# Performance work log

Hardware: AMD Instinct MI355X
Metric: run time of the kernel (lower is better)

Reference implementation:

```python
import jax, jax.numpy as jnp
import numpy as np

N_ATOMS = 100000
N_EDGES = 625000
N_MOL = 1000
EMB_ATOM = 256
EMB_EDGE = 128


def setup_inputs() -> dict:
    key = jax.random.key(0)
    ks = jax.random.split(key, 8)
    h_energy = jax.random.normal(ks[0], (N_ATOMS, EMB_ATOM), dtype=jnp.float32)
    h_forces = jax.random.normal(ks[1], (N_EDGES, EMB_EDGE), dtype=jnp.float32)
    V_st = jax.random.normal(ks[2], (N_EDGES, 3), dtype=jnp.float32)
    idx_t = jax.random.randint(ks[3], (N_EDGES,), 0, N_ATOMS, dtype=jnp.int64)
    batch_idx = jnp.sort(jax.random.randint(ks[4], (N_ATOMS,), 0, N_MOL, dtype=jnp.int64))
    W_energy = jax.random.normal(ks[5], (EMB_ATOM, 1), dtype=jnp.float32) / np.sqrt(EMB_ATOM)
    W_forces = jax.random.normal(ks[6], (EMB_EDGE, 1), dtype=jnp.float32) / np.sqrt(EMB_EDGE)
    b_forces = jnp.zeros((1,), dtype=jnp.float32)
    return {
        "h_energy": h_energy,
        "h_forces": h_forces,
        "V_st": V_st,
        "idx_t": idx_t,
        "batch_idx": batch_idx,
        "W_energy": W_energy,
        "W_forces": W_forces,
        "b_forces": b_forces,
    }


def reference(h_energy, h_forces, V_st, idx_t, batch_idx, W_energy, W_forces, b_forces):
    # Energy head: per-atom linear (bias=False), scatter-sum over molecules.
    e_atom = h_energy @ W_energy                      # [N, 1]
    y = jax.ops.segment_sum(e_atom, batch_idx, num_segments=N_MOL)  # [B, 1]
    y = y[:, 0]                                       # rearrange 'b 1 -> b'
    # Forces head: per-edge linear, scale by unit edge vector V_st,
    # scatter-sum into target atoms idx_t.
    f_edge = (h_forces @ W_forces + b_forces) * V_st  # [E, 3] via broadcast of [E,1]
    force = jax.ops.segment_sum(f_edge, idx_t, num_segments=N_ATOMS)  # [N, 3]
    return y, force
```

## Files before the change

kernel.cpp:

```cpp
#include <hip/hip_runtime.h>

#define N_ATOMS 100000
#define N_EDGES 625000
#define N_MOL   1000
#define EMB_ATOM 256
#define EMB_EDGE 128

typedef float f32x4 __attribute__((ext_vector_type(4)));

__device__ __forceinline__ float dot4(f32x4 a, f32x4 b) {
    return a.x * b.x + a.y * b.y + a.z * b.z + a.w * b.w;
}

#define REP      8
#define YREP_STR 1024
#define FREP_OFF 8192
#define FREP_STR 300000
#define WS_FLOATS (FREP_OFF + REP * FREP_STR)

__global__ __launch_bounds__(256) void zero_kernel(f32x4* __restrict__ p, int n4)
{
    const int i = blockIdx.x * blockDim.x + threadIdx.x;
    if (i < n4) p[i] = (f32x4)(0.f, 0.f, 0.f, 0.f);
}

__global__ __launch_bounds__(256) void merge_kernel(
    const float* __restrict__ ws, float* __restrict__ out)
{
    const int i = blockIdx.x * blockDim.x + threadIdx.x;
    if (i >= 250 + 75000) return;
    const f32x4* w4 = reinterpret_cast<const f32x4*>(ws);
    f32x4*       o4 = reinterpret_cast<f32x4*>(out);
    if (i < 250) {
        f32x4 s = (f32x4)(0.f, 0.f, 0.f, 0.f);
        #pragma unroll
        for (int k = 0; k < REP; ++k) s += w4[i + k * (YREP_STR/4)];
        o4[i] = s;
    } else {
        const int j = i - 250;
        const f32x4* f4 = w4 + FREP_OFF/4;
        f32x4 s = (f32x4)(0.f, 0.f, 0.f, 0.f);
        #pragma unroll
        for (int k = 0; k < REP; ++k) s += f4[j + k * (FREP_STR/4)];
        o4[i] = s;
    }
}

#define FTILES  ((N_EDGES + 15) / 16)
#define FPBLOCKS 1960
#define ETILES  (N_ATOMS / 8)
#define EPBLOCKS 600

__global__ __launch_bounds__(256) void fused_kernel(
    const float* __restrict__ h_energy,
    const float* __restrict__ h_forces,
    const float* __restrict__ V_st,
    const int*   __restrict__ idx_t,
    const int*   __restrict__ batch_idx,
    const float* __restrict__ W_energy,
    const float* __restrict__ W_forces,
    const float* __restrict__ b_forces,
    float*       __restrict__ ws)
{
    const int lane = threadIdx.x & 63;

    if (blockIdx.x < FPBLOCKS) {
        const int wslot = blockIdx.x * 4 + (threadIdx.x >> 6);
        const int slot  = lane >> 3;
        const int sub   = lane & 7;

        const f32x4* wf   = reinterpret_cast<const f32x4*>(W_forces);
        const f32x4* base = reinterpret_cast<const f32x4*>(h_forces);
        float* frep = ws + FREP_OFF + (wslot & (REP-1)) * FREP_STR;

        f32x4 b0 = wf[sub + 0];
        f32x4 b1 = wf[sub + 8];
        f32x4 b2 = wf[sub + 16];
        f32x4 b3 = wf[sub + 24];
        const float bias = b_forces[0];

        for (int tile = wslot; tile < FTILES; tile += FPBLOCKS * 4) {
            #pragma unroll
            for (int g = 0; g < 2; ++g) {
                const int e = tile * 16 + g * 8 + slot;
                float s = 0.f;
                if (e < N_EDGES) {
                    const f32x4* row = base + (size_t)e * 32;
                    f32x4 a0 = __builtin_nontemporal_load(row + sub + 0);
                    f32x4 a1 = __builtin_nontemporal_load(row + sub + 8);
                    f32x4 a2 = __builtin_nontemporal_load(row + sub + 16);
                    f32x4 a3 = __builtin_nontemporal_load(row + sub + 24);
                    s = dot4(a0, b0) + dot4(a1, b1) + dot4(a2, b2) + dot4(a3, b3);
                }
                s += __shfl_xor(s, 1, 64);
                s += __shfl_xor(s, 2, 64);
                s += __shfl_xor(s, 4, 64);
                if (e < N_EDGES && sub < 3) {
                    const int   t = idx_t[e];
                    const float v = V_st[(size_t)e * 3 + sub];
                    atomicAdd(&frep[(size_t)t * 3 + sub], (s + bias) * v);
                }
            }
        }
    } else if (blockIdx.x < FPBLOCKS + EPBLOCKS) {
        const int wslot = (blockIdx.x - FPBLOCKS) * 4 + (threadIdx.x >> 6);
        const int slot  = lane >> 4;
        const int sub   = lane & 15;

        const f32x4* we   = reinterpret_cast<const f32x4*>(W_energy);
        const f32x4* base = reinterpret_cast<const f32x4*>(h_energy);
        float* yrep = ws + (wslot & (REP-1)) * YREP_STR;

        f32x4 b0 = we[sub + 0];
        f32x4 b1 = we[sub + 16];
        f32x4 b2 = we[sub + 32];
        f32x4 b3 = we[sub + 48];

        for (int tile = wslot; tile < ETILES; tile += EPBLOCKS * 4) {
            #pragma unroll
            for (int g = 0; g < 2; ++g) {
                const int a = tile * 8 + g * 4 + slot;
                const f32x4* row = base + (size_t)a * 64;
                f32x4 a0 = __builtin_nontemporal_load(row + sub + 0);
                f32x4 a1 = __builtin_nontemporal_load(row + sub + 16);
                f32x4 a2 = __builtin_nontemporal_load(row + sub + 32);
                f32x4 a3 = __builtin_nontemporal_load(row + sub + 48);
                float s = dot4(a0, b0) + dot4(a1, b1) + dot4(a2, b2) + dot4(a3, b3);

                s += __shfl_xor(s, 1, 64);
                s += __shfl_xor(s, 2, 64);
                s += __shfl_xor(s, 4, 64);
                s += __shfl_xor(s, 8, 64);

                if (sub == 0) atomicAdd(&yrep[batch_idx[a]], s);
            }
        }
    }
}

extern "C" void kernel_launch(void* const* d_in, const int* in_sizes, int n_in,
                              void* d_out, int out_size, void* d_ws, size_t ws_size,
                              hipStream_t stream) {
    const float* h_energy  = (const float*)d_in[0];
    const float* h_forces  = (const float*)d_in[1];
    const float* V_st      = (const float*)d_in[2];
    const int*   idx_t     = (const int*)d_in[3];
    const int*   batch_idx = (const int*)d_in[4];
    const float* W_energy  = (const float*)d_in[5];
    const float* W_forces  = (const float*)d_in[6];
    const float* b_forces  = (const float*)d_in[7];

    float* ws  = (float*)d_ws;
    float* out = (float*)d_out;

    const int zn4 = WS_FLOATS / 4;
    zero_kernel<<<(zn4 + 255) / 256, 256, 0, stream>>>((f32x4*)d_ws, zn4);

    fused_kernel<<<FPBLOCKS + EPBLOCKS, 256, 0, stream>>>(
        h_energy, h_forces, V_st, idx_t, batch_idx,
        W_energy, W_forces, b_forces, ws);

    merge_kernel<<<(75250 + 255) / 256, 256, 0, stream>>>(ws, out);
}
```

Measured before the change: 96.77 us.

## Software-pipeline row loads one tile ahead in both force and energy loops

Restructures both grid-stride loops so each wavefront prefetches the next tile's feature rows, indices and V_st values into registers while it reduces and atomically accumulates the current tile. Out-of-range edges are clamped to a valid row so loads are unconditional. The aim is to hide global memory latency behind the dot-product, shuffle and atomic work. The cost is roughly double the register footprint for row data, which may lower occupancy. Most waves run only about two or three iterations, so there is little to overlap.

```diff
diff --git a/kernel.cpp b/kernel.cpp
--- a/kernel.cpp
+++ b/kernel.cpp
@@ -46,10 +46,12 @@
     }
 }
 
-#define FTILES  ((N_EDGES + 15) / 16)
+#define FTILES   ((N_EDGES + 15) / 16)
 #define FPBLOCKS 1960
-#define ETILES  (N_ATOMS / 8)
+#define FSTRIDE  (FPBLOCKS * 4)
+#define ETILES   (N_ATOMS / 8)
 #define EPBLOCKS 600
+#define ESTRIDE  (EPBLOCKS * 4)
 
 __global__ __launch_bounds__(256) void fused_kernel(
     const float* __restrict__ h_energy,
@@ -79,28 +81,63 @@
         f32x4 b3 = wf[sub + 24];
         const float bias = b_forces[0];
 
-        for (int tile = wslot; tile < FTILES; tile += FPBLOCKS * 4) {
-            #pragma unroll
-            for (int g = 0; g < 2; ++g) {
-                const int e = tile * 16 + g * 8 + slot;
-                float s = 0.f;
-                if (e < N_EDGES) {
-                    const f32x4* row = base + (size_t)e * 32;
-                    f32x4 a0 = __builtin_nontemporal_load(row + sub + 0);
-                    f32x4 a1 = __builtin_nontemporal_load(row + sub + 8);
-                    f32x4 a2 = __builtin_nontemporal_load(row + sub + 16);
-                    f32x4 a3 = __builtin_nontemporal_load(row + sub + 24);
-                    s = dot4(a0, b0) + dot4(a1, b1) + dot4(a2, b2) + dot4(a3, b3);
+        f32x4 c[8]; int ct[2]; float cv[2]; bool cok[2];
+
+        int tile = wslot;
+        {
+            #pragma unroll
+            for (int g = 0; g < 2; ++g) {
+                const int e  = tile * 16 + g * 8 + slot;
+                cok[g] = (e < N_EDGES);
+                const int ec = cok[g] ? e : (N_EDGES - 1);
+                const f32x4* row = base + (size_t)ec * 32;
+                c[g*4+0] = __builtin_nontemporal_load(row + sub + 0);
+                c[g*4+1] = __builtin_nontemporal_load(row + sub + 8);
+                c[g*4+2] = __builtin_nontemporal_load(row + sub + 16);
+                c[g*4+3] = __builtin_nontemporal_load(row + sub + 24);
+                ct[g] = idx_t[ec];
+                cv[g] = V_st[(size_t)ec * 3 + (sub < 3 ? sub : 0)];
+            }
+        }
+
+        for (;;) {
+            const int next     = tile + FSTRIDE;
+            const bool has_next = (next < FTILES);
+
+            f32x4 n[8]; int nt[2]; float nv[2]; bool nok[2];
+            if (has_next) {
+                #pragma unroll
+                for (int g = 0; g < 2; ++g) {
+                    const int e  = next * 16 + g * 8 + slot;
+                    nok[g] = (e < N_EDGES);
+                    const int ec = nok[g] ? e : (N_EDGES - 1);
+                    const f32x4* row = base + (size_t)ec * 32;
+                    n[g*4+0] = __builtin_nontemporal_load(row + sub + 0);
+                    n[g*4+1] = __builtin_nontemporal_load(row + sub + 8);
+                    n[g*4+2] = __builtin_nontemporal_load(row + sub + 16);
+                    n[g*4+3] = __builtin_nontemporal_load(row + sub + 24);
+                    nt[g] = idx_t[ec];
+                    nv[g] = V_st[(size_t)ec * 3 + (sub < 3 ? sub : 0)];
                 }
+            }
+
+            #pragma unroll
+            for (int g = 0; g < 2; ++g) {
+                float s = dot4(c[g*4+0], b0) + dot4(c[g*4+1], b1)
+                        + dot4(c[g*4+2], b2) + dot4(c[g*4+3], b3);
                 s += __shfl_xor(s, 1, 64);
                 s += __shfl_xor(s, 2, 64);
                 s += __shfl_xor(s, 4, 64);
-                if (e < N_EDGES && sub < 3) {
-                    const int   t = idx_t[e];
-                    const float v = V_st[(size_t)e * 3 + sub];
-                    atomicAdd(&frep[(size_t)t * 3 + sub], (s + bias) * v);
-                }
-            }
+                if (cok[g] && sub < 3)
+                    atomicAdd(&frep[(size_t)ct[g] * 3 + sub], (s + bias) * cv[g]);
+            }
+
+            if (!has_next) break;
+            #pragma unroll
+            for (int k = 0; k < 8; ++k) c[k] = n[k];
+            #pragma unroll
+            for (int g = 0; g < 2; ++g) { ct[g] = nt[g]; cv[g] = nv[g]; cok[g] = nok[g]; }
+            tile = next;
         }
     } else if (blockIdx.x < FPBLOCKS + EPBLOCKS) {
         const int wslot = (blockIdx.x - FPBLOCKS) * 4 + (threadIdx.x >> 6);
@@ -116,24 +153,56 @@
         f32x4 b2 = we[sub + 32];
         f32x4 b3 = we[sub + 48];
 
-        for (int tile = wslot; tile < ETILES; tile += EPBLOCKS * 4) {
+        f32x4 c[8]; int cm[2];
+
+        int tile = wslot;
+        {
             #pragma unroll
             for (int g = 0; g < 2; ++g) {
                 const int a = tile * 8 + g * 4 + slot;
                 const f32x4* row = base + (size_t)a * 64;
-                f32x4 a0 = __builtin_nontemporal_load(row + sub + 0);
-                f32x4 a1 = __builtin_nontemporal_load(row + sub + 16);
-                f32x4 a2 = __builtin_nontemporal_load(row + sub + 32);
-                f32x4 a3 = __builtin_nontemporal_load(row + sub + 48);
-                float s = dot4(a0, b0) + dot4(a1, b1) + dot4(a2, b2) + dot4(a3, b3);
-
+                c[g*4+0] = __builtin_nontemporal_load(row + sub + 0);
+                c[g*4+1] = __builtin_nontemporal_load(row + sub + 16);
+                c[g*4+2] = __builtin_nontemporal_load(row + sub + 32);
+                c[g*4+3] = __builtin_nontemporal_load(row + sub + 48);
+                cm[g] = batch_idx[a];
+            }
+        }
+
+        for (;;) {
+            const int next      = tile + ESTRIDE;
+            const bool has_next = (next < ETILES);
+
+            f32x4 n[8]; int nm[2];
+            if (has_next) {
+                #pragma unroll
+                for (int g = 0; g < 2; ++g) {
+                    const int a = next * 8 + g * 4 + slot;
+                    const f32x4* row = base + (size_t)a * 64;
+                    n[g*4+0] = __builtin_nontemporal_load(row + sub + 0);
+                    n[g*4+1] = __builtin_nontemporal_load(row + sub + 16);
+                    n[g*4+2] = __builtin_nontemporal_load(row + sub + 32);
+                    n[g*4+3] = __builtin_nontemporal_load(row + sub + 48);
+                    nm[g] = batch_idx[a];
+                }
+            }
+
+            #pragma unroll
+            for (int g = 0; g < 2; ++g) {
+                float s = dot4(c[g*4+0], b0) + dot4(c[g*4+1], b1)
+                        + dot4(c[g*4+2], b2) + dot4(c[g*4+3], b3);
                 s += __shfl_xor(s, 1, 64);
                 s += __shfl_xor(s, 2, 64);
                 s += __shfl_xor(s, 4, 64);
                 s += __shfl_xor(s, 8, 64);
-
-                if (sub == 0) atomicAdd(&yrep[batch_idx[a]], s);
-            }
+                if (sub == 0) atomicAdd(&yrep[cm[g]], s);
+            }
+
+            if (!has_next) break;
+            #pragma unroll
+            for (int k = 0; k < 8; ++k) c[k] = n[k];
+            cm[0] = nm[0]; cm[1] = nm[1];
+            tile = next;
         }
     }
 }
```

New measurement: 95.96 us. Within noise of the previous version (-0.8%).
